# Optimization experiments

Hardware: AMD Instinct MI355X
Metric: run time of the kernel (lower is better)

Reference implementation:

```python
import jax, jax.numpy as jnp
import numpy as np

N, E, G = 50000, 800000, 512
HD, ED, GD, HID = 128, 64, 64, 128  # h_dim, e_dim, g_dim, hid_dim


def _mlp2(x, W1, b1, W2, b2, last_act):
    # Linear -> ReLU -> Linear (-> optional last activation)
    y = jax.nn.relu(x @ W1 + b1) @ W2 + b2
    return last_act(y) if last_act is not None else y


def setup_inputs() -> dict:
    key = jax.random.key(0)
    ks = list(jax.random.split(key, 24))
    ki = iter(ks)

    def p(shape):
        return (jax.random.normal(next(ki), shape, jnp.float32) * 0.02)

    inp = {
        "h": jax.random.normal(next(ki), (N, HD), jnp.float32),
        "e_index": jax.random.randint(next(ki), (2, E), 0, N),
        "e": jax.random.normal(next(ki), (E, ED), jnp.float32),
        "g": jax.random.normal(next(ki), (G, GD), jnp.float32),
        "batch": jnp.sort(jax.random.randint(next(ki), (N,), 0, G)),
        # fc_m: [2*HD+ED+GD, HID, HID], last_activation=relu
        "W_m1": p((2 * HD + ED + GD, HID)), "b_m1": jnp.zeros((HID,), jnp.float32),
        "W_m2": p((HID, HID)), "b_m2": jnp.zeros((HID,), jnp.float32),
        # fc_m_att: [HID, 1], sigmoid
        "W_ma": p((HID, 1)), "b_ma": jnp.zeros((1,), jnp.float32),
        # fc_e: [HID, ED, ED]
        "W_e1": p((HID, ED)), "b_e1": jnp.zeros((ED,), jnp.float32),
        "W_e2": p((ED, ED)), "b_e2": jnp.zeros((ED,), jnp.float32),
        # fc_h: [HD+HID+GD, HD, HD]
        "W_h1": p((HD + HID + GD, HD)), "b_h1": jnp.zeros((HD,), jnp.float32),
        "W_h2": p((HD, HD)), "b_h2": jnp.zeros((HD,), jnp.float32),
        # fc_h_att: [HD, 1]
        "W_ha": p((HD, 1)), "b_ha": jnp.zeros((1,), jnp.float32),
        # fc_g: [GD+HD, GD, GD]
        "W_g1": p((GD + HD, GD)), "b_g1": jnp.zeros((GD,), jnp.float32),
        "W_g2": p((GD, GD)), "b_g2": jnp.zeros((GD,), jnp.float32),
    }
    return inp


def reference(h, e_index, e, g, batch,
              W_m1, b_m1, W_m2, b_m2, W_ma, b_ma,
              W_e1, b_e1, W_e2, b_e2,
              W_h1, b_h1, W_h2, b_h2, W_ha, b_ha,
              W_g1, b_g1, W_g2, b_g2):
    src, dst = e_index[0], e_index[1]
    e_batch = batch[dst]

    # edge message: concat gathered endpoints + edge feat + gathered global
    m_cat = jnp.concatenate([h[src], h[dst], e, g[e_batch]], axis=1)  # [E, 2HD+ED+GD]
    m = jax.nn.relu(jax.nn.relu(m_cat @ W_m1 + b_m1) @ W_m2 + b_m2)   # [E, HID]
    m_att = jax.nn.sigmoid(m @ W_ma + b_ma)                            # [E, 1]

    e_update = _mlp2(m, W_e1, b_e1, W_e2, b_e2, None)                  # [E, ED]
    e_out = jax.nn.relu(e + e_update)

    m_aggr = jax.ops.segment_sum(m_att * m, dst, num_segments=h.shape[0])  # [N, HID]

    h_cat = jnp.concatenate([h, m_aggr, g[batch]], axis=1)             # [N, HD+HID+GD]
    h_update = _mlp2(h_cat, W_h1, b_h1, W_h2, b_h2, None)
    h_out = jax.nn.relu(h + h_update)                                  # [N, HD]
    h_att = h_out @ W_ha + b_ha                                        # [N, 1]

    h_aggr = jax.ops.segment_sum(h_att * h_out, batch, num_segments=g.shape[0])  # [G, HD]

    g_cat = jnp.concatenate([g, h_aggr], axis=1)                       # [G, GD+HD]
    g_update = _mlp2(g_cat, W_g1, b_g1, W_g2, b_g2, None)
    g_out = jax.nn.relu(g + g_update)

    return (h_out, e_out, g_out)
```

## Files before the change

kernel.cpp:

```cpp
#include <hip/hip_runtime.h>
#include <hip/hip_bf16.h>

#define NN 50000
#define NE 800000
#define NG 512
#define HD 128
#define ED 64
#define GD 64
#define HID 128
#define EB 128

typedef __attribute__((ext_vector_type(8))) short short8;
typedef __attribute__((ext_vector_type(4))) short short4v;
typedef __attribute__((ext_vector_type(4))) float f32x4;
typedef __attribute__((ext_vector_type(16))) float f32x16;

__device__ __forceinline__ short f2bf(float f) {
  union { float f; unsigned u; } v; v.f = f;
  unsigned r = v.u + 0x7fffu + ((v.u >> 16) & 1u);
  return (short)(r >> 16);
}

__device__ __forceinline__ float bf2f(short s) {
  union { unsigned u; float f; } v;
  v.u = ((unsigned)(unsigned short)s) << 16;
  return v.f;
}

__device__ __forceinline__ short8 load_a8(const float* p) {
  const f32x4* q = (const f32x4*)p;
  f32x4 x0 = q[0], x1 = q[1];
  short8 r;
  r[0]=f2bf(x0[0]); r[1]=f2bf(x0[1]); r[2]=f2bf(x0[2]); r[3]=f2bf(x0[3]);
  r[4]=f2bf(x1[0]); r[5]=f2bf(x1[1]); r[6]=f2bf(x1[2]); r[7]=f2bf(x1[3]);
  return r;
}

__device__ __forceinline__ int swz(int row, int col, int rowBytes) {
  int b = row * rowBytes + col * 2;
  b ^= (row & 7) << 4;
  return b >> 1;
}

__global__ void pack_kernel(const float* __restrict__ Wm1, const float* __restrict__ Wm2,
                            const float* __restrict__ We1, const float* __restrict__ We2,
                            const float* __restrict__ Wh1, const float* __restrict__ Wh2,
                            short* __restrict__ out) {
  int gid = blockIdx.x * 256 + threadIdx.x;
  if (gid >= 135168) return;
  const float* W; int Ncol, base, idx;
  if (gid < 49152)       { W = Wm1; Ncol = 128; base = 0;      idx = gid; }
  else if (gid < 65536)  { W = Wm2; Ncol = 128; base = 49152;  idx = gid - 49152; }
  else if (gid < 73728)  { W = We1; Ncol = 64;  base = 65536;  idx = gid - 65536; }
  else if (gid < 77824)  { W = We2; Ncol = 64;  base = 73728;  idx = gid - 73728; }
  else if (gid < 118784) { W = Wh1; Ncol = 128; base = 77824;  idx = gid - 77824; }
  else                   { W = Wh2; Ncol = 128; base = 118784; idx = gid - 118784; }
  int k = idx / Ncol, n = idx % Ncol;
  out[base + (k >> 3) * Ncol * 8 + n * 8 + (k & 7)] = f2bf(W[idx]);
}

__global__ void cast_kernel(const float* __restrict__ h, const float* __restrict__ g,
                            const float* __restrict__ e,
                            short* __restrict__ h_bf, short* __restrict__ g_bf,
                            short* __restrict__ e_bf) {
  int gid = blockIdx.x * 256 + threadIdx.x;
  const int H4 = NN * HD / 4;
  const int G4 = NG * GD / 4;
  const int E4 = NE * ED / 4;
  if (gid < H4) {
    f32x4 v = ((const f32x4*)h)[gid];
    short4v r; r[0]=f2bf(v[0]); r[1]=f2bf(v[1]); r[2]=f2bf(v[2]); r[3]=f2bf(v[3]);
    *(short4v*)(h_bf + gid * 4) = r;
  } else if (gid < H4 + G4) {
    int i = gid - H4;
    f32x4 v = ((const f32x4*)g)[i];
    short4v r; r[0]=f2bf(v[0]); r[1]=f2bf(v[1]); r[2]=f2bf(v[2]); r[3]=f2bf(v[3]);
    *(short4v*)(g_bf + i * 4) = r;
  } else if (gid < H4 + G4 + E4) {
    int i = gid - H4 - G4;
    f32x4 v = ((const f32x4*)e)[i];
    short4v r; r[0]=f2bf(v[0]); r[1]=f2bf(v[1]); r[2]=f2bf(v[2]); r[3]=f2bf(v[3]);
    *(short4v*)(e_bf + i * 4) = r;
  }
}

__global__ void count_kernel(const int* __restrict__ ei, int* __restrict__ deg) {
  int i = blockIdx.x * 256 + threadIdx.x;
  if (i < NE) atomicAdd(&deg[ei[NE + i]], 1);
}

__global__ __launch_bounds__(1024) void scan_kernel(int* __restrict__ deg) {
  __shared__ int psum[1024];
  const int CH = 49;
  int t = threadIdx.x;
  int lo = t * CH, hi = lo + CH; if (hi > NN) hi = NN; if (lo > NN) lo = NN;
  int s = 0;
  for (int i = lo; i < hi; ++i) s += deg[i];
  psum[t] = s;
  __syncthreads();
  for (int d = 1; d < 1024; d <<= 1) {
    int v = (t >= d) ? psum[t - d] : 0;
    __syncthreads();
    psum[t] += v;
    __syncthreads();
  }
  int run = (t == 0) ? 0 : psum[t - 1];
  for (int i = lo; i < hi; ++i) { int v = deg[i]; deg[i] = run; run += v; }
}

__global__ void scatter_kernel(const int* __restrict__ ei, int* __restrict__ off,
                               int* __restrict__ elist) {
  int i = blockIdx.x * 256 + threadIdx.x;
  if (i < NE) {
    int d = ei[NE + i];
    int p = atomicAdd(&off[d], 1);
    elist[p] = i;
  }
}

__global__ __launch_bounds__(256) void edge_kernel(
    const short* __restrict__ h_bf, const int* __restrict__ ei,
    const short* __restrict__ e_bf, const short* __restrict__ g_bf,
    const int* __restrict__ batch, const int* __restrict__ elist,
    const short* __restrict__ pWm1, const float* __restrict__ bm1,
    const short* __restrict__ pWm2, const float* __restrict__ bm2,
    const float* __restrict__ Wma, const float* __restrict__ bma,
    const short* __restrict__ pWe1, const float* __restrict__ be1,
    const short* __restrict__ pWe2, const float* __restrict__ be2,
    float* __restrict__ e_out, float* __restrict__ m_aggr) {
  __shared__ short lds_m[EB * 128];
  __shared__ float att_s[EB];
  __shared__ int sdst[EB];
  __shared__ int seid[EB];
  short* ebuf = lds_m;

  const int tid = threadIdx.x;
  const int w = tid >> 6;
  const int l = tid & 63;
  const int c32 = l & 31;
  const int hi = l >> 5;
  const int eb = blockIdx.x * EB;

  if (tid < EB) {
    int eid = elist[eb + tid];
    seid[tid] = eid;
    sdst[tid] = ei[NE + eid];
  }

  const int myrow = w * 32 + c32;
  const int eidr = elist[eb + myrow];
  const int dstr = ei[NE + eidr];
  const int srcr = ei[eidr];
  const int gbr = batch[dstr];

  f32x16 acc[4];
#pragma unroll
  for (int t = 0; t < 4; ++t) acc[t] = (f32x16)0.0f;

#pragma unroll
  for (int kk = 0; kk < 24; ++kk) {
    short8 a;
    if (kk < 8)
      a = *(const short8*)(h_bf + (size_t)srcr * HD + kk * 16 + hi * 8);
    else if (kk < 16)
      a = *(const short8*)(h_bf + (size_t)dstr * HD + (kk - 8) * 16 + hi * 8);
    else if (kk < 20)
      a = *(const short8*)(e_bf + (size_t)eidr * ED + (kk - 16) * 16 + hi * 8);
    else
      a = *(const short8*)(g_bf + (size_t)gbr * GD + (kk - 20) * 16 + hi * 8);
    const short* bp = pWm1 + (size_t)(kk * 2 + hi) * (HID * 8) + c32 * 8;
#pragma unroll
    for (int t = 0; t < 4; ++t) {
      short8 b = *(const short8*)(bp + t * 32 * 8);
      acc[t] = __builtin_amdgcn_mfma_f32_32x32x16_bf16(a, b, acc[t], 0, 0, 0);
    }
  }

#pragma unroll
  for (int t = 0; t < 4; ++t) {
    float bb = bm1[t * 32 + c32];
#pragma unroll
    for (int q = 0; q < 16; ++q) {
      int row = w * 32 + (q & 3) + 8 * (q >> 2) + 4 * hi;
      float y = fmaxf(acc[t][q] + bb, 0.f);
      lds_m[swz(row, t * 32 + c32, 256)] = f2bf(y);
    }
  }

  f32x16 acc2[4];
#pragma unroll
  for (int t = 0; t < 4; ++t) acc2[t] = (f32x16)0.0f;

#pragma unroll
  for (int ks = 0; ks < 8; ++ks) {
    short8 a = *(const short8*)&lds_m[swz(w * 32 + c32, ks * 16 + hi * 8, 256)];
    const short* bp = pWm2 + (size_t)(ks * 2 + hi) * (HID * 8) + c32 * 8;
#pragma unroll
    for (int t = 0; t < 4; ++t) {
      short8 b = *(const short8*)(bp + t * 32 * 8);
      acc2[t] = __builtin_amdgcn_mfma_f32_32x32x16_bf16(a, b, acc2[t], 0, 0, 0);
    }
  }

  float p[16];
#pragma unroll
  for (int q = 0; q < 16; ++q) p[q] = 0.f;

#pragma unroll
  for (int t = 0; t < 4; ++t) {
    float bb = bm2[t * 32 + c32];
    float wv = Wma[t * 32 + c32];
#pragma unroll
    for (int q = 0; q < 16; ++q) {
      int row = w * 32 + (q & 3) + 8 * (q >> 2) + 4 * hi;
      float y = fmaxf(acc2[t][q] + bb, 0.f);
      lds_m[swz(row, t * 32 + c32, 256)] = f2bf(y);
      p[q] += y * wv;
    }
  }

#pragma unroll
  for (int s = 1; s <= 16; s <<= 1) {
#pragma unroll
    for (int q = 0; q < 16; ++q) p[q] += __shfl_xor(p[q], s, 64);
  }
  {
    float bma0 = bma[0];
    if (c32 == 0) {
#pragma unroll
      for (int q = 0; q < 16; ++q) {
        int row = w * 32 + (q & 3) + 8 * (q >> 2) + 4 * hi;
        att_s[row] = 1.f / (1.f + __expf(-(p[q] + bma0)));
      }
    }
  }

  f32x16 acc3[2];
#pragma unroll
  for (int t = 0; t < 2; ++t) acc3[t] = (f32x16)0.0f;

#pragma unroll
  for (int ks = 0; ks < 8; ++ks) {
    short8 a = *(const short8*)&lds_m[swz(w * 32 + c32, ks * 16 + hi * 8, 256)];
    const short* bp = pWe1 + (size_t)(ks * 2 + hi) * (ED * 8) + c32 * 8;
#pragma unroll
    for (int t = 0; t < 2; ++t) {
      short8 b = *(const short8*)(bp + t * 32 * 8);
      acc3[t] = __builtin_amdgcn_mfma_f32_32x32x16_bf16(a, b, acc3[t], 0, 0, 0);
    }
  }

  __syncthreads();

  {
    int col = tid & 127;
    int r0 = (tid >> 7) * 64;
    int cur = sdst[r0];
    float sum = 0.f;
    bool first = true;
#pragma unroll 1
    for (int r = r0; r < r0 + 64; ++r) {
      int d = sdst[r];
      float v = bf2f(lds_m[swz(r, col, 256)]) * att_s[r];
      if (d != cur) {
        if (first) atomicAdd(&m_aggr[(size_t)cur * HID + col], sum);
        else m_aggr[(size_t)cur * HID + col] = sum;
        first = false; cur = d; sum = v;
      } else {
        sum += v;
      }
    }
    atomicAdd(&m_aggr[(size_t)cur * HID + col], sum);
  }

  __syncthreads();

#pragma unroll
  for (int t = 0; t < 2; ++t) {
    float bb = be1[t * 32 + c32];
#pragma unroll
    for (int q = 0; q < 16; ++q) {
      int row = w * 32 + (q & 3) + 8 * (q >> 2) + 4 * hi;
      float y = fmaxf(acc3[t][q] + bb, 0.f);
      ebuf[swz(row, t * 32 + c32, 128)] = f2bf(y);
    }
  }

  f32x16 acc4[2];
#pragma unroll
  for (int t = 0; t < 2; ++t) acc4[t] = (f32x16)0.0f;

#pragma unroll
  for (int ks = 0; ks < 4; ++ks) {
    short8 a = *(const short8*)&ebuf[swz(w * 32 + c32, ks * 16 + hi * 8, 128)];
    const short* bp = pWe2 + (size_t)(ks * 2 + hi) * (ED * 8) + c32 * 8;
#pragma unroll
    for (int t = 0; t < 2; ++t) {
      short8 b = *(const short8*)(bp + t * 32 * 8);
      acc4[t] = __builtin_amdgcn_mfma_f32_32x32x16_bf16(a, b, acc4[t], 0, 0, 0);
    }
  }

#pragma unroll
  for (int t = 0; t < 2; ++t) {
    float bb = be2[t * 32 + c32];
#pragma unroll
    for (int q = 0; q < 16; ++q) {
      int row = w * 32 + (q & 3) + 8 * (q >> 2) + 4 * hi;
      int eid = seid[row];
      int col = t * 32 + c32;
      float v = bf2f(e_bf[(size_t)eid * ED + col]) + acc4[t][q] + bb;
      e_out[(size_t)eid * ED + col] = fmaxf(v, 0.f);
    }
  }
}

__global__ __launch_bounds__(256) void node_kernel(
    const float* __restrict__ h, const short* __restrict__ h_bf,
    const float* __restrict__ m_aggr, const short* __restrict__ g_bf,
    const int* __restrict__ batch,
    const short* __restrict__ pWh1, const float* __restrict__ bh1,
    const short* __restrict__ pWh2, const float* __restrict__ bh2,
    const float* __restrict__ Wha, const float* __restrict__ bha,
    float* __restrict__ h_out, float* __restrict__ h_aggr) {
  __shared__ short lds_y[4][16 * 128];
  __shared__ int sbat[64];

  const int wave = threadIdx.x >> 6;
  const int lane = threadIdx.x & 63;
  const int row16 = lane & 15;
  const int quad = lane >> 4;
  const int nbase = blockIdx.x * 64 + wave * 16;

  int nA = nbase + row16;
  int nAc = nA < NN ? nA : NN - 1;
  int gbA = batch[nAc];
  if (quad == 0) sbat[wave * 16 + row16] = (nA < NN) ? gbA : -1;

  short8 afr[10];
  {
    const short* s0 = h_bf + (size_t)nAc * HD;
    const float* s1 = m_aggr + (size_t)nAc * HID;
    const short* s2 = g_bf + (size_t)gbA * GD;
#pragma unroll
    for (int c = 0; c < 4; ++c) afr[c] = *(const short8*)(s0 + c * 32 + quad * 8);
#pragma unroll
    for (int c = 0; c < 4; ++c) afr[4 + c] = load_a8(s1 + c * 32 + quad * 8);
    afr[8] = *(const short8*)(s2 + quad * 8);
    afr[9] = *(const short8*)(s2 + 32 + quad * 8);
  }

  f32x4 acc[8];
#pragma unroll
  for (int t = 0; t < 8; ++t) acc[t] = (f32x4)0.0f;
#pragma unroll
  for (int c = 0; c < 10; ++c) {
    const short* bp = pWh1 + (size_t)(c * 4 + quad) * HD * 8 + row16 * 8;
#pragma unroll
    for (int t = 0; t < 8; ++t) {
      short8 b = *(const short8*)(bp + t * 16 * 8);
      acc[t] = __builtin_amdgcn_mfma_f32_16x16x32_bf16(afr[c], b, acc[t], 0, 0, 0);
    }
  }
#pragma unroll
  for (int t = 0; t < 8; ++t) {
    float b1 = bh1[t * 16 + row16];
#pragma unroll
    for (int r = 0; r < 4; ++r) {
      float y = fmaxf(acc[t][r] + b1, 0.f);
      lds_y[wave][swz(quad * 4 + r, t * 16 + row16, 256)] = f2bf(y);
    }
  }

  f32x4 acc2[8];
#pragma unroll
  for (int t = 0; t < 8; ++t) acc2[t] = (f32x4)0.0f;
#pragma unroll
  for (int c = 0; c < 4; ++c) {
    short8 a = *(const short8*)&lds_y[wave][swz(row16, c * 32 + quad * 8, 256)];
    const short* bp = pWh2 + (size_t)(c * 4 + quad) * HD * 8 + row16 * 8;
#pragma unroll
    for (int t = 0; t < 8; ++t) {
      short8 b = *(const short8*)(bp + t * 16 * 8);
      acc2[t] = __builtin_amdgcn_mfma_f32_16x16x32_bf16(a, b, acc2[t], 0, 0, 0);
    }
  }

  float hval[8][4];
  int nS[4];
#pragma unroll
  for (int r = 0; r < 4; ++r) nS[r] = nbase + quad * 4 + r;
#pragma unroll
  for (int t = 0; t < 8; ++t) {
    float b2 = bh2[t * 16 + row16];
#pragma unroll
    for (int r = 0; r < 4; ++r) {
      float v = 0.f;
      if (nS[r] < NN) {
        v = h[(size_t)nS[r] * HD + t * 16 + row16] + acc2[t][r] + b2;
        v = fmaxf(v, 0.f);
        h_out[(size_t)nS[r] * HD + t * 16 + row16] = v;
      }
      hval[t][r] = v;
    }
  }

  float part[4] = {0.f, 0.f, 0.f, 0.f};
#pragma unroll
  for (int t = 0; t < 8; ++t) {
    float w = Wha[t * 16 + row16];
#pragma unroll
    for (int r = 0; r < 4; ++r) part[r] += hval[t][r] * w;
  }
#pragma unroll
  for (int s = 1; s < 16; s <<= 1) {
#pragma unroll
    for (int r = 0; r < 4; ++r) part[r] += __shfl_xor(part[r], s, 64);
  }
  float bha0 = bha[0];
#pragma unroll
  for (int t = 0; t < 8; ++t)
#pragma unroll
    for (int r = 0; r < 4; ++r)
      lds_y[wave][swz(quad * 4 + r, t * 16 + row16, 256)] =
          f2bf((part[r] + bha0) * hval[t][r]);

  __syncthreads();

  {
    int col = threadIdx.x & 127;
    int r0 = (threadIdx.x >> 7) * 32;
    int cur = sbat[r0];
    float sum = 0.f;
    bool first = true;
#pragma unroll 1
    for (int r = r0; r < r0 + 32; ++r) {
      int d = sbat[r];
      float v = bf2f(lds_y[r >> 4][swz(r & 15, col, 256)]);
      if (d != cur) {
        if (cur >= 0) {
          if (first) atomicAdd(&h_aggr[(size_t)cur * HD + col], sum);
          else h_aggr[(size_t)cur * HD + col] = sum;
        }
        first = false; cur = d; sum = v;
      } else {
        sum += v;
      }
    }
    if (cur >= 0) atomicAdd(&h_aggr[(size_t)cur * HD + col], sum);
  }
}

__global__ void g_kernel(const float* __restrict__ g, const float* __restrict__ h_aggr,
                         const float* __restrict__ Wg1, const float* __restrict__ bg1,
                         const float* __restrict__ Wg2, const float* __restrict__ bg2,
                         float* __restrict__ g_out) {
  __shared__ float cat[192];
  __shared__ float y1[64];
  int r = blockIdx.x;
  int t = threadIdx.x;
  cat[t] = g[(size_t)r * GD + t];
  cat[64 + t] = h_aggr[(size_t)r * HD + t];
  cat[128 + t] = h_aggr[(size_t)r * HD + 64 + t];
  __syncthreads();
  float a = bg1[t];
  for (int k = 0; k < 192; ++k) a += cat[k] * Wg1[k * 64 + t];
  y1[t] = fmaxf(a, 0.f);
  __syncthreads();
  float b = bg2[t];
  for (int k = 0; k < 64; ++k) b += y1[k] * Wg2[k * 64 + t];
  float v = g[(size_t)r * GD + t] + b;
  g_out[(size_t)r * GD + t] = fmaxf(v, 0.f);
}

extern "C" void kernel_launch(void* const* d_in, const int* in_sizes, int n_in,
                              void* d_out, int out_size, void* d_ws, size_t ws_size,
                              hipStream_t stream) {
  const float* h = (const float*)d_in[0];
  const int* ei = (const int*)d_in[1];
  const float* e = (const float*)d_in[2];
  const float* g = (const float*)d_in[3];
  const int* batch = (const int*)d_in[4];
  const float* Wm1 = (const float*)d_in[5];
  const float* bm1 = (const float*)d_in[6];
  const float* Wm2 = (const float*)d_in[7];
  const float* bm2 = (const float*)d_in[8];
  const float* Wma = (const float*)d_in[9];
  const float* bma = (const float*)d_in[10];
  const float* We1 = (const float*)d_in[11];
  const float* be1 = (const float*)d_in[12];
  const float* We2 = (const float*)d_in[13];
  const float* be2 = (const float*)d_in[14];
  const float* Wh1 = (const float*)d_in[15];
  const float* bh1 = (const float*)d_in[16];
  const float* Wh2 = (const float*)d_in[17];
  const float* bh2 = (const float*)d_in[18];
  const float* Wha = (const float*)d_in[19];
  const float* bha = (const float*)d_in[20];
  const float* Wg1 = (const float*)d_in[21];
  const float* bg1 = (const float*)d_in[22];
  const float* Wg2 = (const float*)d_in[23];
  const float* bg2 = (const float*)d_in[24];

  float* out = (float*)d_out;
  float* h_out = out;
  float* e_out = out + (size_t)NN * HD;
  float* g_out = e_out + (size_t)NE * ED;

  char* ws = (char*)d_ws;
  float* m_aggr = (float*)ws;
  float* h_aggr = (float*)(ws + 25600000);
  short* packed = (short*)(ws + 25862144);
  int* deg      = (int*)(ws + 26132480);
  int* elist    = (int*)(ws + 26332480);
  short* h_bf   = (short*)(ws + 29532480);
  short* g_bf   = (short*)(ws + 42332480);
  short* e_bf   = (short*)(ws + 42398016);
  short* pWm1 = packed;
  short* pWm2 = packed + 49152;
  short* pWe1 = packed + 65536;
  short* pWe2 = packed + 73728;
  short* pWh1 = packed + 77824;
  short* pWh2 = packed + 118784;

  hipMemsetAsync(m_aggr, 0, (size_t)NN * HID * 4, stream);
  hipMemsetAsync(h_aggr, 0, (size_t)NG * HD * 4, stream);
  hipMemsetAsync(deg, 0, (size_t)NN * 4, stream);

  pack_kernel<<<(135168 + 255) / 256, 256, 0, stream>>>(Wm1, Wm2, We1, We2, Wh1, Wh2, packed);
  cast_kernel<<<(14408192 + 255) / 256, 256, 0, stream>>>(h, g, e, h_bf, g_bf, e_bf);
  count_kernel<<<(NE + 255) / 256, 256, 0, stream>>>(ei, deg);
  scan_kernel<<<1, 1024, 0, stream>>>(deg);
  scatter_kernel<<<(NE + 255) / 256, 256, 0, stream>>>(ei, deg, elist);

  edge_kernel<<<NE / EB, 256, 0, stream>>>(h_bf, ei, e_bf, g_bf, batch, elist,
                                           pWm1, bm1, pWm2, bm2, Wma, bma,
                                           pWe1, be1, pWe2, be2, e_out, m_aggr);

  node_kernel<<<(NN + 63) / 64, 256, 0, stream>>>(h, h_bf, m_aggr, g_bf, batch,
                                                  pWh1, bh1, pWh2, bh2, Wha, bha,
                                                  h_out, h_aggr);

  g_kernel<<<NG, 64, 0, stream>>>(g, h_aggr, Wg1, bg1, Wg2, bg2, g_out);
}
```

Measured before the change: 714.3 us.

## Split edge GEMM into halves, cache edge residual in LDS, fuse degree count

```diff
diff --git a/kernel.cpp b/kernel.cpp
--- a/kernel.cpp
+++ b/kernel.cpp
@@ -12,6 +12,7 @@
 
 typedef __attribute__((ext_vector_type(8))) short short8;
 typedef __attribute__((ext_vector_type(4))) short short4v;
+typedef __attribute__((ext_vector_type(2))) float f32x2;
 typedef __attribute__((ext_vector_type(4))) float f32x4;
 typedef __attribute__((ext_vector_type(16))) float f32x16;
 
@@ -60,9 +61,9 @@
 }
 
 __global__ void cast_kernel(const float* __restrict__ h, const float* __restrict__ g,
-                            const float* __restrict__ e,
+                            const float* __restrict__ e, const int* __restrict__ ei,
                             short* __restrict__ h_bf, short* __restrict__ g_bf,
-                            short* __restrict__ e_bf) {
+                            short* __restrict__ e_bf, int* __restrict__ deg) {
   int gid = blockIdx.x * 256 + threadIdx.x;
   const int H4 = NN * HD / 4;
   const int G4 = NG * GD / 4;
@@ -81,12 +82,10 @@
     f32x4 v = ((const f32x4*)e)[i];
     short4v r; r[0]=f2bf(v[0]); r[1]=f2bf(v[1]); r[2]=f2bf(v[2]); r[3]=f2bf(v[3]);
     *(short4v*)(e_bf + i * 4) = r;
-  }
-}
-
-__global__ void count_kernel(const int* __restrict__ ei, int* __restrict__ deg) {
-  int i = blockIdx.x * 256 + threadIdx.x;
-  if (i < NE) atomicAdd(&deg[ei[NE + i]], 1);
+  } else if (gid < H4 + G4 + E4 + NE) {
+    int i = gid - H4 - G4 - E4;
+    atomicAdd(&deg[ei[NE + i]], 1);
+  }
 }
 
 __global__ __launch_bounds__(1024) void scan_kernel(int* __restrict__ deg) {
@@ -118,7 +117,7 @@
   }
 }
 
-__global__ __launch_bounds__(256) void edge_kernel(
+__global__ __launch_bounds__(256, 3) void edge_kernel(
     const short* __restrict__ h_bf, const int* __restrict__ ei,
     const short* __restrict__ e_bf, const short* __restrict__ g_bf,
     const int* __restrict__ batch, const int* __restrict__ elist,
@@ -129,6 +128,7 @@
     const short* __restrict__ pWe2, const float* __restrict__ be2,
     float* __restrict__ e_out, float* __restrict__ m_aggr) {
   __shared__ short lds_m[EB * 128];
+  __shared__ short eres_lds[EB * 64];
   __shared__ float att_s[EB];
   __shared__ int sdst[EB];
   __shared__ int seid[EB];
@@ -153,37 +153,40 @@
   const int srcr = ei[eidr];
   const int gbr = batch[dstr];
 
-  f32x16 acc[4];
-#pragma unroll
-  for (int t = 0; t < 4; ++t) acc[t] = (f32x16)0.0f;
-
-#pragma unroll
-  for (int kk = 0; kk < 24; ++kk) {
-    short8 a;
-    if (kk < 8)
-      a = *(const short8*)(h_bf + (size_t)srcr * HD + kk * 16 + hi * 8);
-    else if (kk < 16)
-      a = *(const short8*)(h_bf + (size_t)dstr * HD + (kk - 8) * 16 + hi * 8);
-    else if (kk < 20)
-      a = *(const short8*)(e_bf + (size_t)eidr * ED + (kk - 16) * 16 + hi * 8);
-    else
-      a = *(const short8*)(g_bf + (size_t)gbr * GD + (kk - 20) * 16 + hi * 8);
-    const short* bp = pWm1 + (size_t)(kk * 2 + hi) * (HID * 8) + c32 * 8;
-#pragma unroll
-    for (int t = 0; t < 4; ++t) {
-      short8 b = *(const short8*)(bp + t * 32 * 8);
-      acc[t] = __builtin_amdgcn_mfma_f32_32x32x16_bf16(a, b, acc[t], 0, 0, 0);
-    }
-  }
-
-#pragma unroll
-  for (int t = 0; t < 4; ++t) {
-    float bb = bm1[t * 32 + c32];
-#pragma unroll
-    for (int q = 0; q < 16; ++q) {
-      int row = w * 32 + (q & 3) + 8 * (q >> 2) + 4 * hi;
-      float y = fmaxf(acc[t][q] + bb, 0.f);
-      lds_m[swz(row, t * 32 + c32, 256)] = f2bf(y);
+#pragma unroll 1
+  for (int half = 0; half < 2; ++half) {
+    f32x16 acc[2];
+    acc[0] = (f32x16)0.0f; acc[1] = (f32x16)0.0f;
+    const short* bbase = pWm1 + (size_t)hi * (HID * 8) + (half * 64 + c32) * 8;
+#pragma unroll
+    for (int kk = 0; kk < 24; ++kk) {
+      short8 a;
+      if (kk < 8)
+        a = *(const short8*)(h_bf + (size_t)srcr * HD + kk * 16 + hi * 8);
+      else if (kk < 16)
+        a = *(const short8*)(h_bf + (size_t)dstr * HD + (kk - 8) * 16 + hi * 8);
+      else if (kk < 20)
+        a = *(const short8*)(e_bf + (size_t)eidr * ED + (kk - 16) * 16 + hi * 8);
+      else
+        a = *(const short8*)(g_bf + (size_t)gbr * GD + (kk - 20) * 16 + hi * 8);
+      if (half == 0 && kk >= 16 && kk < 20)
+        *(short8*)&eres_lds[swz(myrow, (kk - 16) * 16 + hi * 8, 128)] = a;
+      const short* bp = bbase + (size_t)kk * 2 * (HID * 8);
+      short8 b0 = *(const short8*)(bp);
+      short8 b1 = *(const short8*)(bp + 32 * 8);
+      acc[0] = __builtin_amdgcn_mfma_f32_32x32x16_bf16(a, b0, acc[0], 0, 0, 0);
+      acc[1] = __builtin_amdgcn_mfma_f32_32x32x16_bf16(a, b1, acc[1], 0, 0, 0);
+    }
+#pragma unroll
+    for (int tt = 0; tt < 2; ++tt) {
+      int col = half * 64 + tt * 32 + c32;
+      float bb = bm1[col];
+#pragma unroll
+      for (int q = 0; q < 16; ++q) {
+        int row = w * 32 + (q & 3) + 8 * (q >> 2) + 4 * hi;
+        float y = fmaxf(acc[tt][q] + bb, 0.f);
+        lds_m[swz(row, col, 256)] = f2bf(y);
+      }
     }
   }
 
@@ -253,24 +256,33 @@
   __syncthreads();
 
   {
-    int col = tid & 127;
-    int r0 = (tid >> 7) * 64;
+    int cp = tid & 63;
+    int r0 = (tid >> 6) * 32;
     int cur = sdst[r0];
-    float sum = 0.f;
+    float s0 = 0.f, s1 = 0.f;
     bool first = true;
 #pragma unroll 1
-    for (int r = r0; r < r0 + 64; ++r) {
+    for (int r = r0; r < r0 + 32; ++r) {
       int d = sdst[r];
-      float v = bf2f(lds_m[swz(r, col, 256)]) * att_s[r];
+      unsigned u = *(const unsigned*)&lds_m[swz(r, cp * 2, 256)];
+      float av = att_s[r];
+      float v0 = bf2f((short)(u & 0xffffu)) * av;
+      float v1 = bf2f((short)(u >> 16)) * av;
       if (d != cur) {
-        if (first) atomicAdd(&m_aggr[(size_t)cur * HID + col], sum);
-        else m_aggr[(size_t)cur * HID + col] = sum;
-        first = false; cur = d; sum = v;
+        if (first) {
+          atomicAdd(&m_aggr[(size_t)cur * HID + cp * 2], s0);
+          atomicAdd(&m_aggr[(size_t)cur * HID + cp * 2 + 1], s1);
+        } else {
+          f32x2 st; st[0] = s0; st[1] = s1;
+          *(f32x2*)&m_aggr[(size_t)cur * HID + cp * 2] = st;
+        }
+        first = false; cur = d; s0 = v0; s1 = v1;
       } else {
-        sum += v;
+        s0 += v0; s1 += v1;
       }
     }
-    atomicAdd(&m_aggr[(size_t)cur * HID + col], sum);
+    atomicAdd(&m_aggr[(size_t)cur * HID + cp * 2], s0);
+    atomicAdd(&m_aggr[(size_t)cur * HID + cp * 2 + 1], s1);
   }
 
   __syncthreads();
@@ -309,7 +321,8 @@
       int row = w * 32 + (q & 3) + 8 * (q >> 2) + 4 * hi;
       int eid = seid[row];
       int col = t * 32 + c32;
-      float v = bf2f(e_bf[(size_t)eid * ED + col]) + acc4[t][q] + bb;
+      float res = bf2f(eres_lds[swz(row, col, 128)]);
+      float v = res + acc4[t][q] + bb;
       e_out[(size_t)eid * ED + col] = fmaxf(v, 0.f);
     }
   }
@@ -528,8 +541,7 @@
   hipMemsetAsync(deg, 0, (size_t)NN * 4, stream);
 
   pack_kernel<<<(135168 + 255) / 256, 256, 0, stream>>>(Wm1, Wm2, We1, We2, Wh1, Wh2, packed);
-  cast_kernel<<<(14408192 + 255) / 256, 256, 0, stream>>>(h, g, e, h_bf, g_bf, e_bf);
-  count_kernel<<<(NE + 255) / 256, 256, 0, stream>>>(ei, deg);
+  cast_kernel<<<(15208192 + 255) / 256, 256, 0, stream>>>(h, g, e, ei, h_bf, g_bf, e_bf, deg);
   scan_kernel<<<1, 1024, 0, stream>>>(deg);
   scatter_kernel<<<(NE + 255) / 256, 256, 0, stream>>>(ei, deg, elist);
 
```

Result: slower. 902.1 us (+26.3%).
